# Performance work log

Hardware: AMD Instinct MI355X
Metric: run time of the kernel (lower is better)

The kernel has to match this reference:

```python
import jax, jax.numpy as jnp
import numpy as np

DIM = 2048
CTX_DIM = 4096
NUM_HEADS = 16
HEAD_DIM = DIM // NUM_HEADS
EPS = 1e-6


def _rms_norm(x, weight, eps=EPS):
    # RMSNorm over last dim with learned weight (native dtype path for fp32)
    var = jnp.mean(jnp.square(x), axis=-1, keepdims=True)
    return x * jax.lax.rsqrt(var + eps) * weight


def setup_inputs() -> dict:
    key = jax.random.key(0)
    ks = jax.random.split(key, 12)
    B, L, S = 1, 8192, 512
    sd_q = 1.0 / np.sqrt(DIM)
    sd_c = 1.0 / np.sqrt(CTX_DIM)
    return {
        "x": jax.random.normal(ks[0], (B, L, DIM), dtype=jnp.float32),
        "context": jax.random.normal(ks[1], (B, S, CTX_DIM), dtype=jnp.float32),
        "Wq": jax.random.normal(ks[2], (DIM, DIM), dtype=jnp.float32) * sd_q,
        "bq": jax.random.normal(ks[3], (DIM,), dtype=jnp.float32) * 0.01,
        "Wk": jax.random.normal(ks[4], (CTX_DIM, DIM), dtype=jnp.float32) * sd_c,
        "bk": jax.random.normal(ks[5], (DIM,), dtype=jnp.float32) * 0.01,
        "Wv": jax.random.normal(ks[6], (CTX_DIM, DIM), dtype=jnp.float32) * sd_c,
        "bv": jax.random.normal(ks[7], (DIM,), dtype=jnp.float32) * 0.01,
        "Wo": jax.random.normal(ks[8], (DIM, DIM), dtype=jnp.float32) * sd_q,
        "bo": jax.random.normal(ks[9], (DIM,), dtype=jnp.float32) * 0.01,
        "g_q": jnp.ones((DIM,), dtype=jnp.float32),
        "g_k": jnp.ones((DIM,), dtype=jnp.float32),
    }


def reference(x, context, Wq, bq, Wk, bk, Wv, bv, Wo, bo, g_q, g_k):
    B, L, C = x.shape
    S = context.shape[1]
    # QKV projections + RMSNorm on Q,K (over full model dim, pre head split)
    q = _rms_norm(x @ Wq + bq, g_q)           # [B, L, C]
    k = _rms_norm(context @ Wk + bk, g_k)     # [B, S, C]
    v = context @ Wv + bv                     # [B, S, C]
    # split heads
    q = q.reshape(B, L, NUM_HEADS, HEAD_DIM)
    k = k.reshape(B, S, NUM_HEADS, HEAD_DIM)
    v = v.reshape(B, S, NUM_HEADS, HEAD_DIM)
    # non-causal SDPA
    scale = 1.0 / np.sqrt(HEAD_DIM)
    scores = jnp.einsum("blhd,bshd->bhls", q, k) * scale
    probs = jax.nn.softmax(scores, axis=-1)
    attn = jnp.einsum("bhls,bshd->blhd", probs, v).reshape(B, L, C)
    return attn @ Wo + bo
```

## Files before the change

kernel.cpp:

```cpp
#include <hip/hip_runtime.h>
#include <hip/hip_bf16.h>
#include <stdint.h>

#define L_SEQ 8192
#define S_SEQ 512
#define DIM   2048
#define CTX   4096
#define NH    16
#define HD    128

typedef __bf16 bf16_t;
typedef bf16_t bf16x8 __attribute__((ext_vector_type(8)));
typedef float  f32x4_t __attribute__((ext_vector_type(4)));
typedef float  f32x16_t __attribute__((ext_vector_type(16)));

__device__ __forceinline__ ushort f2b(float f) {
  bf16_t h = (bf16_t)f;
  return __builtin_bit_cast(ushort, h);
}
__device__ __forceinline__ uint32_t pk2(float a, float b) {
  return (uint32_t)f2b(a) | ((uint32_t)f2b(b) << 16);
}
__device__ __forceinline__ float b2f(ushort u) {
  union { uint32_t u; float f; } v; v.u = ((uint32_t)u) << 16;
  return v.f;
}
__device__ __forceinline__ void gll16(const ushort* g, ushort* l) {
  __builtin_amdgcn_global_load_lds((const __attribute__((address_space(1))) void*)g,
                                   (__attribute__((address_space(3))) void*)l, 16, 0, 0);
}
#define SBAR() __builtin_amdgcn_sched_barrier(0)

__global__ __launch_bounds__(256) void k_prep(const float* __restrict__ x,
                                              const float* __restrict__ ctx,
                                              const float* __restrict__ Wq,
                                              const float* __restrict__ Wk,
                                              const float* __restrict__ Wv,
                                              const float* __restrict__ Wo,
                                              const float* __restrict__ gq,
                                              const float* __restrict__ gk,
                                              ushort* __restrict__ xb,
                                              ushort* __restrict__ ctxb,
                                              ushort* __restrict__ wqt,
                                              ushort* __restrict__ wkt,
                                              ushort* __restrict__ wvt,
                                              ushort* __restrict__ wot,
                                              float* __restrict__ g2) {
  const int b = blockIdx.x;
  const int tid = threadIdx.x;
  if (b == 33792) {
    const int d = tid * 8;
#pragma unroll
    for (int j = 0; j < 8; j++) g2[d + j] = gq[d + j] * gk[d + j] * 0.08838834764831843f;
    return;
  }
  if (b < 9216) {
    const float* src; ushort* dst; size_t i;
    if (b < 8192) { src = x;   dst = xb;   i = ((size_t)b * 256 + tid) * 8; }
    else          { src = ctx; dst = ctxb; i = ((size_t)(b - 8192) * 256 + tid) * 8; }
    float4 a = *(const float4*)(src + i);
    float4 c = *(const float4*)(src + i + 4);
    uint4 r;
    r.x = pk2(a.x, a.y); r.y = pk2(a.z, a.w);
    r.z = pk2(c.x, c.y); r.w = pk2(c.z, c.w);
    *(uint4*)(dst + i) = r;
    return;
  }
  __shared__ float t[32][33];
  const float* src; ushort* dst; int K, ti;
  if (b < 13312)      { src = Wq; dst = wqt; K = DIM; ti = b - 9216; }
  else if (b < 21504) { src = Wk; dst = wkt; K = CTX; ti = b - 13312; }
  else if (b < 29696) { src = Wv; dst = wvt; K = CTX; ti = b - 21504; }
  else                { src = Wo; dst = wot; K = DIM; ti = b - 29696; }
  const int n0 = (ti & 63) * 32, k0 = (ti >> 6) * 32;
  const int tx = tid & 31, ty = tid >> 5;
#pragma unroll
  for (int i = 0; i < 4; i++)
    t[ty + 8 * i][tx] = src[(size_t)(k0 + ty + 8 * i) * DIM + n0 + tx];
  __syncthreads();
#pragma unroll
  for (int i = 0; i < 4; i++)
    dst[(size_t)(n0 + ty + 8 * i) * K + k0 + tx] = f2b(t[tx][ty + 8 * i]);
}

__global__ __launch_bounds__(256) void k_knorm(const ushort* __restrict__ kraw,
                                               ushort* __restrict__ kb) {
  const int row = blockIdx.x, tid = threadIdx.x;
  uint4 v = *(const uint4*)(kraw + (size_t)row * DIM + tid * 8);
  const uint32_t* vu = (const uint32_t*)&v;
  float f[8];
#pragma unroll
  for (int i = 0; i < 4; i++) {
    f[2 * i]     = b2f((ushort)(vu[i] & 0xffffu));
    f[2 * i + 1] = b2f((ushort)(vu[i] >> 16));
  }
  float s = 0.f;
#pragma unroll
  for (int i = 0; i < 8; i++) s += f[i] * f[i];
#pragma unroll
  for (int off = 32; off; off >>= 1) s += __shfl_down(s, off);
  __shared__ float wsum[4];
  __shared__ float rtot;
  if ((tid & 63) == 0) wsum[tid >> 6] = s;
  __syncthreads();
  if (tid == 0)
    rtot = rsqrtf((wsum[0] + wsum[1] + wsum[2] + wsum[3]) * (1.0f / DIM) + 1e-6f);
  __syncthreads();
  const float rms = rtot;
  ushort r[8];
#pragma unroll
  for (int i = 0; i < 8; i++) r[i] = f2b(f[i] * rms);
  *(uint4*)(kb + (size_t)row * DIM + tid * 8) = *(uint4*)r;
}

template <int OUT_MODE>
__global__ __launch_bounds__(512, 2) void k_gemm256(const ushort* __restrict__ A,
                                                    const ushort* __restrict__ Bt,
                                                    const float* __restrict__ bias,
                                                    void* __restrict__ outp,
                                                    float* __restrict__ qpart,
                                                    int M, int N, int K) {
  __shared__ __align__(16) ushort lds[65536];
  const int tid = threadIdx.x;
  const int l = tid & 63, wid = tid >> 6;
  const int wm = wid >> 2, wn = wid & 3;
  const int lr = l & 15, lq = l >> 4;

  const int nwg = gridDim.x * gridDim.y;
  const int bid = blockIdx.y * gridDim.x + blockIdx.x;
  const int swz = (bid & 7) * (nwg >> 3) + (bid >> 3);
  const int m0 = (swz / gridDim.x) * 256, n0 = (swz % gridDim.x) * 256;

  f32x4_t acc[8][4];
#pragma unroll
  for (int i = 0; i < 8; i++)
#pragma unroll
    for (int j = 0; j < 4; j++) acc[i][j] = f32x4_t{0.f, 0.f, 0.f, 0.f};

  const int srow = l >> 3;
  const int schunk = ((l & 7) ^ (srow & 7)) * 8;
  auto stage = [&](int buf, int tile, int mat, int h) {
    const ushort* gp = mat ? Bt : A;
    const int rn0 = mat ? n0 : m0;
    const size_t r0 = (size_t)(rn0 + h * 128 + wid * 8 + srow);
    const ushort* g0 = gp + r0 * K + tile * 64 + schunk;
    ushort* l0 = &lds[buf * 32768 + mat * 16384 + (h * 128 + wid * 8) * 64];
    gll16(g0, l0);
    gll16(g0 + (size_t)64 * K, l0 + 64 * 64);
  };

  auto rdA = [&](int buf, int mf, int ks) -> bf16x8 {
    const int R = wm * 128 + mf * 16 + lr;
    return *(const bf16x8*)(&lds[buf * 32768 + R * 64 + (((ks * 4 + lq) ^ (R & 7)) * 8)]);
  };
  auto rdB = [&](int buf, int nf, int ks) -> bf16x8 {
    const int R = wn * 64 + nf * 16 + lr;
    return *(const bf16x8*)(&lds[buf * 32768 + 16384 + R * 64 + (((ks * 4 + lq) ^ (R & 7)) * 8)]);
  };

  const int NT = K >> 6;
  const int NI = NT >> 1;

  stage(0, 0, 0, 0); stage(0, 0, 0, 1); stage(0, 0, 1, 0); stage(0, 0, 1, 1);
  stage(1, 1, 0, 0); stage(1, 1, 0, 1); stage(1, 1, 1, 0); stage(1, 1, 1, 1);
  asm volatile("s_waitcnt vmcnt(8)" ::: "memory");
  SBAR();
  __builtin_amdgcn_s_barrier();
  SBAR();

  bf16x8 a[4][2], a2[4][2], b[2][2], b2[2][2];
  for (int i = 0; i < NI; i++) {
    const bool pf = (i + 1 < NI);
#pragma unroll
    for (int half = 0; half < 2; half++) {
      const int buf = half;
      const int st = 2 * i + 2 + half;
#pragma unroll
      for (int mf = 0; mf < 4; mf++) { a[mf][0] = rdA(buf, mf, 0); a[mf][1] = rdA(buf, mf, 1); }
#pragma unroll
      for (int nf = 0; nf < 2; nf++) { b[nf][0] = rdB(buf, nf, 0); b[nf][1] = rdB(buf, nf, 1); }
      SBAR();
      __builtin_amdgcn_s_barrier();
      asm volatile("s_waitcnt lgkmcnt(0)" ::: "memory");
      SBAR();
      __builtin_amdgcn_s_setprio(1);
#pragma unroll
      for (int mf = 0; mf < 4; mf++)
#pragma unroll
        for (int nf = 0; nf < 2; nf++) {
          acc[mf][nf] = __builtin_amdgcn_mfma_f32_16x16x32_bf16(a[mf][0], b[nf][0], acc[mf][nf], 0, 0, 0);
          acc[mf][nf] = __builtin_amdgcn_mfma_f32_16x16x32_bf16(a[mf][1], b[nf][1], acc[mf][nf], 0, 0, 0);
        }
      __builtin_amdgcn_s_setprio(0);
      SBAR();
      __builtin_amdgcn_s_barrier();
      SBAR();
#pragma unroll
      for (int mf = 0; mf < 4; mf++) { a2[mf][0] = rdA(buf, mf + 4, 0); a2[mf][1] = rdA(buf, mf + 4, 1); }
      SBAR();
      __builtin_amdgcn_s_barrier();
      asm volatile("s_waitcnt lgkmcnt(0)" ::: "memory");
      SBAR();
      __builtin_amdgcn_s_setprio(1);
#pragma unroll
      for (int mf = 0; mf < 4; mf++)
#pragma unroll
        for (int nf = 0; nf < 2; nf++) {
          acc[mf + 4][nf] = __builtin_amdgcn_mfma_f32_16x16x32_bf16(a2[mf][0], b[nf][0], acc[mf + 4][nf], 0, 0, 0);
          acc[mf + 4][nf] = __builtin_amdgcn_mfma_f32_16x16x32_bf16(a2[mf][1], b[nf][1], acc[mf + 4][nf], 0, 0, 0);
        }
      __builtin_amdgcn_s_setprio(0);
      SBAR();
      __builtin_amdgcn_s_barrier();
      SBAR();
#pragma unroll
      for (int nf = 0; nf < 2; nf++) { b2[nf][0] = rdB(buf, nf + 2, 0); b2[nf][1] = rdB(buf, nf + 2, 1); }
      if (pf) { stage(buf, st, 0, 0); stage(buf, st, 0, 1); }
      SBAR();
      __builtin_amdgcn_s_barrier();
      asm volatile("s_waitcnt lgkmcnt(0)" ::: "memory");
      SBAR();
      __builtin_amdgcn_s_setprio(1);
#pragma unroll
      for (int mf = 0; mf < 4; mf++)
#pragma unroll
        for (int nf = 0; nf < 2; nf++) {
          acc[mf + 4][nf + 2] = __builtin_amdgcn_mfma_f32_16x16x32_bf16(a2[mf][0], b2[nf][0], acc[mf + 4][nf + 2], 0, 0, 0);
          acc[mf + 4][nf + 2] = __builtin_amdgcn_mfma_f32_16x16x32_bf16(a2[mf][1], b2[nf][1], acc[mf + 4][nf + 2], 0, 0, 0);
        }
      __builtin_amdgcn_s_setprio(0);
      SBAR();
      __builtin_amdgcn_s_barrier();
      SBAR();
      if (pf) {
        stage(buf, st, 1, 0); stage(buf, st, 1, 1);
        asm volatile("s_waitcnt vmcnt(8)" ::: "memory");
      } else if (half == 0) {
        asm volatile("s_waitcnt vmcnt(0)" ::: "memory");
      }
      SBAR();
      __builtin_amdgcn_s_barrier();
      SBAR();
      __builtin_amdgcn_s_setprio(1);
#pragma unroll
      for (int mf = 0; mf < 4; mf++)
#pragma unroll
        for (int nf = 0; nf < 2; nf++) {
          acc[mf][nf + 2] = __builtin_amdgcn_mfma_f32_16x16x32_bf16(a[mf][0], b2[nf][0], acc[mf][nf + 2], 0, 0, 0);
          acc[mf][nf + 2] = __builtin_amdgcn_mfma_f32_16x16x32_bf16(a[mf][1], b2[nf][1], acc[mf][nf + 2], 0, 0, 0);
        }
      __builtin_amdgcn_s_setprio(0);
      SBAR();
      __builtin_amdgcn_s_barrier();
      SBAR();
    }
  }

  float bvs[4];
#pragma unroll
  for (int nf = 0; nf < 4; nf++) bvs[nf] = bias[n0 + wn * 64 + nf * 16 + lr];
#pragma unroll
  for (int nf = 0; nf < 4; nf++) {
    const int col = n0 + wn * 64 + nf * 16 + lr;
#pragma unroll
    for (int mf = 0; mf < 8; mf++) {
#pragma unroll
      for (int r = 0; r < 4; r++) {
        const int row = m0 + wm * 128 + mf * 16 + lq * 4 + r;
        const float v = acc[mf][nf][r] + bvs[nf];
        if constexpr (OUT_MODE == 0)
          ((float*)outp)[(size_t)row * N + col] = v;
        else
          ((ushort*)outp)[(size_t)row * N + col] = f2b(v);
      }
    }
  }
  if constexpr (OUT_MODE == 1) {
    const int slot = (n0 >> 8) * 4 + wn;
#pragma unroll
    for (int mf = 0; mf < 8; mf++) {
#pragma unroll
      for (int r = 0; r < 4; r++) {
        float s = 0.f;
#pragma unroll
        for (int nf = 0; nf < 4; nf++) {
          const float v = acc[mf][nf][r] + bvs[nf];
          s += v * v;
        }
        s += __shfl_xor(s, 1); s += __shfl_xor(s, 2);
        s += __shfl_xor(s, 4); s += __shfl_xor(s, 8);
        if (lr == 0)
          qpart[(size_t)(m0 + wm * 128 + mf * 16 + lq * 4 + r) * 32 + slot] = s;
      }
    }
  }
}

__global__ __launch_bounds__(256) void k_gemmkv(const ushort* __restrict__ A,
                                                const ushort* __restrict__ Bt,
                                                const float* __restrict__ biasK,
                                                const float* __restrict__ biasV,
                                                ushort* __restrict__ outK,
                                                ushort* __restrict__ outVt) {
  __shared__ __align__(16) ushort As[4][128 * 32];
  __shared__ __align__(16) ushort Bs[4][64 * 32];
  const int tid = threadIdx.x;
  const int l = tid & 63, wid = tid >> 6;
  const int wr = wid >> 1, wc = wid & 1;
  const int lr = l & 15, lq = l >> 4;
  const int K = CTX, M = S_SEQ;

  const int bid = blockIdx.x;
  const int swz = (bid & 7) * 32 + (bid >> 3);
  const int n0 = (swz >> 2) * 64, m0 = (swz & 3) * 128;

  f32x4_t acc[4][2];
#pragma unroll
  for (int i = 0; i < 4; i++)
#pragma unroll
    for (int j = 0; j < 2; j++) acc[i][j] = f32x4_t{0.f, 0.f, 0.f, 0.f};

  const int srow = l >> 2;
  const int schunk = ((l & 3) ^ ((srow >> 1) & 3)) * 8;
  const ushort* gA = A  + (size_t)(m0 + srow) * K + schunk;
  const ushort* gB = Bt + (size_t)(n0 + wid * 16 + srow) * K + schunk;

  auto stage = [&](int buf, int kt) {
    const int ko = kt * 32;
    gll16(gA + (size_t)(wid * 16) * K + ko,      &As[buf][(wid * 16) * 32]);
    gll16(gA + (size_t)(64 + wid * 16) * K + ko, &As[buf][(64 + wid * 16) * 32]);
    gll16(gB + ko,                               &Bs[buf][(wid * 16) * 32]);
  };
  auto rdA = [&](int buf, int mi) -> bf16x8 {
    const int R = wr * 64 + mi * 16 + lr;
    return *(const bf16x8*)(&As[buf][R * 32 + ((lq ^ ((R >> 1) & 3)) * 8)]);
  };
  auto rdB = [&](int buf, int ni) -> bf16x8 {
    const int R = wc * 32 + ni * 16 + lr;
    return *(const bf16x8*)(&Bs[buf][R * 32 + ((lq ^ ((R >> 1) & 3)) * 8)]);
  };

  const int NT = K >> 5;
  stage(0, 0); stage(1, 1); stage(2, 2);
  for (int t = 0; t < NT; t++) {
    const int cur = t & 3;
    if (t + 3 < NT) { stage((t + 3) & 3, t + 3); asm volatile("s_waitcnt vmcnt(9)" ::: "memory"); }
    else if (t + 2 < NT) { asm volatile("s_waitcnt vmcnt(6)" ::: "memory"); }
    else if (t + 1 < NT) { asm volatile("s_waitcnt vmcnt(3)" ::: "memory"); }
    else                 { asm volatile("s_waitcnt vmcnt(0)" ::: "memory"); }
    SBAR();
    __builtin_amdgcn_s_barrier();
    SBAR();

    bf16x8 af[4], bfr[2];
#pragma unroll
    for (int mi = 0; mi < 4; mi++) af[mi] = rdA(cur, mi);
#pragma unroll
    for (int ni = 0; ni < 2; ni++) bfr[ni] = rdB(cur, ni);
    __builtin_amdgcn_s_setprio(1);
#pragma unroll
    for (int mi = 0; mi < 4; mi++)
#pragma unroll
      for (int ni = 0; ni < 2; ni++)
        acc[mi][ni] = __builtin_amdgcn_mfma_f32_16x16x32_bf16(af[mi], bfr[ni], acc[mi][ni], 0, 0, 0);
    __builtin_amdgcn_s_setprio(0);
    SBAR();
    __builtin_amdgcn_s_barrier();
    SBAR();
  }

  if (n0 < DIM) {
#pragma unroll
    for (int mi = 0; mi < 4; mi++) {
#pragma unroll
      for (int ni = 0; ni < 2; ni++) {
        const int col = n0 + wc * 32 + ni * 16 + lr;
        const float bv = biasK[col];
#pragma unroll
        for (int r = 0; r < 4; r++) {
          const int row = m0 + wr * 64 + mi * 16 + lq * 4 + r;
          outK[(size_t)row * DIM + col] = f2b(acc[mi][ni][r] + bv);
        }
      }
    }
  } else {
    ushort* ldst = &As[0][0];
    __syncthreads();
#pragma unroll
    for (int mi = 0; mi < 4; mi++) {
#pragma unroll
      for (int ni = 0; ni < 2; ni++) {
        const int ccol = wc * 32 + ni * 16 + lr;
        const float bv = biasV[n0 - DIM + ccol];
#pragma unroll
        for (int r = 0; r < 4; r++) {
          const int crow = wr * 64 + mi * 16 + lq * 4 + r;
          ldst[ccol * 128 + crow] = f2b(acc[mi][ni][r] + bv);
        }
      }
    }
    __syncthreads();
    const int c = tid >> 2, j0 = (tid & 3) * 32;
    ushort* dst = outVt + (size_t)(n0 - DIM + c) * M + m0 + j0;
#pragma unroll
    for (int k2 = 0; k2 < 4; k2++)
      *(uint4*)(dst + k2 * 8) = *(const uint4*)(ldst + c * 128 + j0 + k2 * 8);
  }
}

__global__ __launch_bounds__(256) void k_attn(const ushort* __restrict__ Qraw,
                                              const ushort* __restrict__ Kb,
                                              const ushort* __restrict__ Vt,
                                              const float* __restrict__ qpart,
                                              const float* __restrict__ g2,
                                              ushort* __restrict__ Ob) {
  __shared__ __align__(16) ushort smem[16384];
  ushort* Ks = smem;
  ushort* Vs = smem + 64 * 128;

  const int tid = threadIdx.x;
  const int l = tid & 63, wid = tid >> 6;
  const int lo = l & 31, hi = l >> 5;

  const int bid = blockIdx.x;
  const int swz = (bid & 7) * 128 + (bid >> 3);
  const int h = swz >> 6;
  const int q0 = (swz & 63) * 128 + wid * 32;

  bf16x8 qf[8];
  {
    float ssum = 0.f;
    const float* pp = qpart + (size_t)(q0 + lo) * 32;
#pragma unroll
    for (int i = 0; i < 8; i++) {
      float4 t = *(const float4*)(pp + i * 4);
      ssum += t.x + t.y + t.z + t.w;
    }
    const float qs = rsqrtf(ssum * (1.0f / DIM) + 1e-6f);
    const ushort* qp = Qraw + (size_t)(q0 + lo) * DIM + h * HD + hi * 8;
    const float* gp = g2 + h * HD + hi * 8;
#pragma unroll
    for (int ds = 0; ds < 8; ds++) {
      union { uint4 u; ushort us[8]; } rw;
      rw.u = *(const uint4*)(qp + ds * 16);
      float4 ga_ = *(const float4*)(gp + ds * 16);
      float4 gb_ = *(const float4*)(gp + ds * 16 + 4);
      union { uint32_t w[4]; bf16x8 v; } ov;
      ov.w[0] = pk2(b2f(rw.us[0]) * qs * ga_.x, b2f(rw.us[1]) * qs * ga_.y);
      ov.w[1] = pk2(b2f(rw.us[2]) * qs * ga_.z, b2f(rw.us[3]) * qs * ga_.w);
      ov.w[2] = pk2(b2f(rw.us[4]) * qs * gb_.x, b2f(rw.us[5]) * qs * gb_.y);
      ov.w[3] = pk2(b2f(rw.us[6]) * qs * gb_.z, b2f(rw.us[7]) * qs * gb_.w);
      qf[ds] = ov.v;
    }
  }

  f32x16_t o[4] = {};
  float m_run = -1e30f, l_run = 0.f;

  for (int kvb = 0; kvb < S_SEQ / 64; kvb++) {
    __syncthreads();
#pragma unroll
    for (int i = 0; i < 4; i++) {
      const int c = i * 256 + tid, row = c >> 4, cs = c & 15;
      gll16(Kb + (size_t)(kvb * 64 + row) * DIM + h * HD + ((cs ^ (row & 7)) * 8),
            Ks + c * 8);
    }
#pragma unroll
    for (int i = 0; i < 4; i++) {
      const int c = i * 256 + tid, row = c >> 3, cs = c & 7;
      gll16(Vt + (size_t)(h * HD + row) * S_SEQ + kvb * 64 + ((cs ^ (row & 7)) * 8),
            Vs + c * 8);
    }
    __syncthreads();

    f32x16_t sA = {}, sB = {};
#pragma unroll
    for (int ds = 0; ds < 8; ds++) {
      const int ch = ((hi + ds * 2) ^ (lo & 7)) * 8;
      bf16x8 kA = *(const bf16x8*)(Ks + lo * 128 + ch);
      bf16x8 kB = *(const bf16x8*)(Ks + (32 + lo) * 128 + ch);
      sA = __builtin_amdgcn_mfma_f32_32x32x16_bf16(kA, qf[ds], sA, 0, 0, 0);
      sB = __builtin_amdgcn_mfma_f32_32x32x16_bf16(kB, qf[ds], sB, 0, 0, 0);
    }

    float p[32];
#pragma unroll
    for (int i = 0; i < 16; i++) { p[i] = sA[i]; p[16 + i] = sB[i]; }
    float pm = p[0];
#pragma unroll
    for (int i = 1; i < 32; i++) pm = fmaxf(pm, p[i]);
    pm = fmaxf(pm, __shfl_xor(pm, 32));
    const float mn = fmaxf(m_run, pm);
    const float corr = __expf(m_run - mn);
    m_run = mn;
    float ps = 0.f;
#pragma unroll
    for (int i = 0; i < 32; i++) { p[i] = __expf(p[i] - mn); ps += p[i]; }
    ps += __shfl_xor(ps, 32);
    l_run = l_run * corr + ps;
#pragma unroll
    for (int nt = 0; nt < 4; nt++) o[nt] *= corr;

    uint32_t c[16];
#pragma unroll
    for (int j = 0; j < 16; j++) c[j] = pk2(p[2 * j], p[2 * j + 1]);
    bf16x8 pf[4];
#pragma unroll
    for (int s = 0; s < 4; s++) {
      const uint32_t ca = c[4 * s], cb = c[4 * s + 1], cc = c[4 * s + 2], cd = c[4 * s + 3];
      const uint32_t sa = __shfl_xor(ca, 32), sb = __shfl_xor(cb, 32);
      const uint32_t sc = __shfl_xor(cc, 32), sd = __shfl_xor(cd, 32);
      union { uint32_t u[4]; bf16x8 v; } f;
      f.u[0] = hi ? sc : ca; f.u[1] = hi ? sd : cb;
      f.u[2] = hi ? cc : sa; f.u[3] = hi ? cd : sb;
      pf[s] = f.v;
    }

#pragma unroll
    for (int nt = 0; nt < 4; nt++) {
      const int vrow = nt * 32 + lo;
#pragma unroll
      for (int s = 0; s < 4; s++) {
        bf16x8 vf = *(const bf16x8*)(Vs + vrow * 64 + (((s * 2 + hi) ^ (lo & 7)) * 8));
        o[nt] = __builtin_amdgcn_mfma_f32_32x32x16_bf16(vf, pf[s], o[nt], 0, 0, 0);
      }
    }
  }

  const float inv = 1.0f / l_run;
#pragma unroll
  for (int nt = 0; nt < 4; nt++) o[nt] *= inv;

  __syncthreads();
  float* tb = (float*)smem + wid * (32 * 33);
  const int q2 = l >> 1, dh = (l & 1) * 16;
#pragma unroll
  for (int nt = 0; nt < 4; nt++) {
#pragma unroll
    for (int r = 0; r < 16; r++)
      tb[lo * 33 + ((r & 3) + 8 * (r >> 2) + 4 * hi)] = o[nt][r];
    asm volatile("s_waitcnt lgkmcnt(0)" ::: "memory");
    SBAR();
    ushort tmp[16];
#pragma unroll
    for (int j = 0; j < 16; j++) tmp[j] = f2b(tb[q2 * 33 + dh + j]);
    asm volatile("s_waitcnt lgkmcnt(0)" ::: "memory");
    SBAR();
    const size_t oaddr = (size_t)(q0 + q2) * DIM + h * HD + nt * 32 + dh;
    *(uint4*)(Ob + oaddr) = *(uint4*)tmp;
    *(uint4*)(Ob + oaddr + 8) = *(uint4*)(tmp + 8);
  }
}

extern "C" void kernel_launch(void* const* d_in, const int* in_sizes, int n_in,
                              void* d_out, int out_size, void* d_ws, size_t ws_size,
                              hipStream_t stream) {
  const float* x   = (const float*)d_in[0];
  const float* ctx = (const float*)d_in[1];
  const float* Wq  = (const float*)d_in[2];
  const float* bq  = (const float*)d_in[3];
  const float* Wk  = (const float*)d_in[4];
  const float* bk  = (const float*)d_in[5];
  const float* Wv  = (const float*)d_in[6];
  const float* bv  = (const float*)d_in[7];
  const float* Wo  = (const float*)d_in[8];
  const float* bo  = (const float*)d_in[9];
  const float* gq  = (const float*)d_in[10];
  const float* gk  = (const float*)d_in[11];

  char* ws = (char*)d_ws;
  ushort* wqt    = (ushort*)(ws);
  ushort* wkt    = (ushort*)(ws + 8388608);
  ushort* wvt    = (ushort*)(ws + 25165824);
  ushort* wot    = (ushort*)(ws + 41943040);
  ushort* ctxb   = (ushort*)(ws + 50331648);
  float*  g2     = (float*)(ws + 54558720);
  float*  qpart  = (float*)(ws + 56623104);
  ushort* kb     = (ushort*)(ws + 83886080);
  ushort* vt     = (ushort*)(ws + 85983232);
  ushort* xb     = (ushort*)(ws + 88080384);
  ushort* kraw   = (ushort*)(ws + 88080384);
  ushort* attnb  = (ushort*)(ws + 88080384);
  ushort* qraw   = (ushort*)(ws + 121634816);

  k_prep<<<33793, 256, 0, stream>>>(x, ctx, Wq, Wk, Wv, Wo, gq, gk,
                                    xb, ctxb, wqt, wkt, wvt, wot, g2);
  k_gemm256<1><<<dim3(DIM / 256, L_SEQ / 256), 512, 0, stream>>>(xb, wqt, bq, qraw, qpart, L_SEQ, DIM, DIM);
  k_gemmkv<<<256, 256, 0, stream>>>(ctxb, wkt, bk, bv, kraw, vt);
  k_knorm<<<S_SEQ, 256, 0, stream>>>(kraw, kb);
  k_attn<<<L_SEQ / 128 * NH, 256, 0, stream>>>(qraw, kb, vt, qpart, g2, attnb);
  k_gemm256<0><<<dim3(DIM / 256, L_SEQ / 256), 512, 0, stream>>>(attnb, wot, bo, d_out, nullptr, L_SEQ, DIM, DIM);
}
```

Measured before the change: 312.5 us.

## Rework GEMM K-loop staging, deepen KV GEMM pipeline, add lazy softmax rescale

The main Q/O GEMM drops the two-tiles-per-iteration loop with two in-flight buffers and uses a simple per-tile double-buffered loop. The next tile's four staging chunks are spread across the compute phases, and the waitcnt now covers only the first chunk. The KV GEMM ring buffer grows from 4 to 6 LDS slots with a prefetch depth of 5, with waitcnt values adjusted to match. Flash attention skips the running-max update and output rescale when the new block max stays within 8 of the current max, avoiding exp and multiply work. The risks are less load latency hiding in the main GEMM, higher LDS use lowering occupancy in the KV GEMM, and a possible race: chunks staged into nxt are only guarded by a vmcnt(2) wait, so the next iteration may read data that has not fully arrived.

```diff
diff --git a/kernel.cpp b/kernel.cpp
--- a/kernel.cpp
+++ b/kernel.cpp
@@ -159,101 +159,87 @@
   };
 
   const int NT = K >> 6;
-  const int NI = NT >> 1;
-
   stage(0, 0, 0, 0); stage(0, 0, 0, 1); stage(0, 0, 1, 0); stage(0, 0, 1, 1);
-  stage(1, 1, 0, 0); stage(1, 1, 0, 1); stage(1, 1, 1, 0); stage(1, 1, 1, 1);
-  asm volatile("s_waitcnt vmcnt(8)" ::: "memory");
-  SBAR();
-  __builtin_amdgcn_s_barrier();
-  SBAR();
 
   bf16x8 a[4][2], a2[4][2], b[2][2], b2[2][2];
-  for (int i = 0; i < NI; i++) {
-    const bool pf = (i + 1 < NI);
-#pragma unroll
-    for (int half = 0; half < 2; half++) {
-      const int buf = half;
-      const int st = 2 * i + 2 + half;
-#pragma unroll
-      for (int mf = 0; mf < 4; mf++) { a[mf][0] = rdA(buf, mf, 0); a[mf][1] = rdA(buf, mf, 1); }
-#pragma unroll
-      for (int nf = 0; nf < 2; nf++) { b[nf][0] = rdB(buf, nf, 0); b[nf][1] = rdB(buf, nf, 1); }
-      SBAR();
-      __builtin_amdgcn_s_barrier();
-      asm volatile("s_waitcnt lgkmcnt(0)" ::: "memory");
-      SBAR();
-      __builtin_amdgcn_s_setprio(1);
-#pragma unroll
-      for (int mf = 0; mf < 4; mf++)
-#pragma unroll
-        for (int nf = 0; nf < 2; nf++) {
-          acc[mf][nf] = __builtin_amdgcn_mfma_f32_16x16x32_bf16(a[mf][0], b[nf][0], acc[mf][nf], 0, 0, 0);
-          acc[mf][nf] = __builtin_amdgcn_mfma_f32_16x16x32_bf16(a[mf][1], b[nf][1], acc[mf][nf], 0, 0, 0);
-        }
-      __builtin_amdgcn_s_setprio(0);
-      SBAR();
-      __builtin_amdgcn_s_barrier();
-      SBAR();
-#pragma unroll
-      for (int mf = 0; mf < 4; mf++) { a2[mf][0] = rdA(buf, mf + 4, 0); a2[mf][1] = rdA(buf, mf + 4, 1); }
-      SBAR();
-      __builtin_amdgcn_s_barrier();
-      asm volatile("s_waitcnt lgkmcnt(0)" ::: "memory");
-      SBAR();
-      __builtin_amdgcn_s_setprio(1);
-#pragma unroll
-      for (int mf = 0; mf < 4; mf++)
-#pragma unroll
-        for (int nf = 0; nf < 2; nf++) {
-          acc[mf + 4][nf] = __builtin_amdgcn_mfma_f32_16x16x32_bf16(a2[mf][0], b[nf][0], acc[mf + 4][nf], 0, 0, 0);
-          acc[mf + 4][nf] = __builtin_amdgcn_mfma_f32_16x16x32_bf16(a2[mf][1], b[nf][1], acc[mf + 4][nf], 0, 0, 0);
-        }
-      __builtin_amdgcn_s_setprio(0);
-      SBAR();
-      __builtin_amdgcn_s_barrier();
-      SBAR();
-#pragma unroll
-      for (int nf = 0; nf < 2; nf++) { b2[nf][0] = rdB(buf, nf + 2, 0); b2[nf][1] = rdB(buf, nf + 2, 1); }
-      if (pf) { stage(buf, st, 0, 0); stage(buf, st, 0, 1); }
-      SBAR();
-      __builtin_amdgcn_s_barrier();
-      asm volatile("s_waitcnt lgkmcnt(0)" ::: "memory");
-      SBAR();
-      __builtin_amdgcn_s_setprio(1);
-#pragma unroll
-      for (int mf = 0; mf < 4; mf++)
-#pragma unroll
-        for (int nf = 0; nf < 2; nf++) {
-          acc[mf + 4][nf + 2] = __builtin_amdgcn_mfma_f32_16x16x32_bf16(a2[mf][0], b2[nf][0], acc[mf + 4][nf + 2], 0, 0, 0);
-          acc[mf + 4][nf + 2] = __builtin_amdgcn_mfma_f32_16x16x32_bf16(a2[mf][1], b2[nf][1], acc[mf + 4][nf + 2], 0, 0, 0);
-        }
-      __builtin_amdgcn_s_setprio(0);
-      SBAR();
-      __builtin_amdgcn_s_barrier();
-      SBAR();
-      if (pf) {
-        stage(buf, st, 1, 0); stage(buf, st, 1, 1);
-        asm volatile("s_waitcnt vmcnt(8)" ::: "memory");
-      } else if (half == 0) {
-        asm volatile("s_waitcnt vmcnt(0)" ::: "memory");
-      }
-      SBAR();
-      __builtin_amdgcn_s_barrier();
-      SBAR();
-      __builtin_amdgcn_s_setprio(1);
-#pragma unroll
-      for (int mf = 0; mf < 4; mf++)
-#pragma unroll
-        for (int nf = 0; nf < 2; nf++) {
-          acc[mf][nf + 2] = __builtin_amdgcn_mfma_f32_16x16x32_bf16(a[mf][0], b2[nf][0], acc[mf][nf + 2], 0, 0, 0);
-          acc[mf][nf + 2] = __builtin_amdgcn_mfma_f32_16x16x32_bf16(a[mf][1], b2[nf][1], acc[mf][nf + 2], 0, 0, 0);
-        }
-      __builtin_amdgcn_s_setprio(0);
-      SBAR();
-      __builtin_amdgcn_s_barrier();
-      SBAR();
-    }
+  for (int kt = 0; kt < NT; kt++) {
+    const int cur = kt & 1, nxt = cur ^ 1;
+    const bool pf = (kt + 1 < NT);
+    if (pf) { stage(nxt, kt + 1, 0, 0); asm volatile("s_waitcnt vmcnt(2)" ::: "memory"); }
+    else    { asm volatile("s_waitcnt vmcnt(0)" ::: "memory"); }
+    SBAR();
+    __builtin_amdgcn_s_barrier();
+    SBAR();
+#pragma unroll
+    for (int mf = 0; mf < 4; mf++) { a[mf][0] = rdA(cur, mf, 0); a[mf][1] = rdA(cur, mf, 1); }
+#pragma unroll
+    for (int nf = 0; nf < 2; nf++) { b[nf][0] = rdB(cur, nf, 0); b[nf][1] = rdB(cur, nf, 1); }
+    __builtin_amdgcn_s_setprio(1);
+#pragma unroll
+    for (int mf = 0; mf < 4; mf++)
+#pragma unroll
+      for (int nf = 0; nf < 2; nf++) {
+        acc[mf][nf] = __builtin_amdgcn_mfma_f32_16x16x32_bf16(a[mf][0], b[nf][0], acc[mf][nf], 0, 0, 0);
+        acc[mf][nf] = __builtin_amdgcn_mfma_f32_16x16x32_bf16(a[mf][1], b[nf][1], acc[mf][nf], 0, 0, 0);
+      }
+    __builtin_amdgcn_s_setprio(0);
+    SBAR();
+    __builtin_amdgcn_s_barrier();
+    SBAR();
+#pragma unroll
+    for (int mf = 0; mf < 4; mf++) { a2[mf][0] = rdA(cur, mf + 4, 0); a2[mf][1] = rdA(cur, mf + 4, 1); }
+    if (pf) stage(nxt, kt + 1, 0, 1);
+    SBAR();
+    __builtin_amdgcn_s_barrier();
+    SBAR();
+    __builtin_amdgcn_s_setprio(1);
+#pragma unroll
+    for (int mf = 0; mf < 4; mf++)
+#pragma unroll
+      for (int nf = 0; nf < 2; nf++) {
+        acc[mf + 4][nf] = __builtin_amdgcn_mfma_f32_16x16x32_bf16(a2[mf][0], b[nf][0], acc[mf + 4][nf], 0, 0, 0);
+        acc[mf + 4][nf] = __builtin_amdgcn_mfma_f32_16x16x32_bf16(a2[mf][1], b[nf][1], acc[mf + 4][nf], 0, 0, 0);
+      }
+    __builtin_amdgcn_s_setprio(0);
+    SBAR();
+    __builtin_amdgcn_s_barrier();
+    SBAR();
+#pragma unroll
+    for (int nf = 0; nf < 2; nf++) { b2[nf][0] = rdB(cur, nf + 2, 0); b2[nf][1] = rdB(cur, nf + 2, 1); }
+    if (pf) stage(nxt, kt + 1, 1, 0);
+    SBAR();
+    __builtin_amdgcn_s_barrier();
+    SBAR();
+    __builtin_amdgcn_s_setprio(1);
+#pragma unroll
+    for (int mf = 0; mf < 4; mf++)
+#pragma unroll
+      for (int nf = 0; nf < 2; nf++) {
+        acc[mf + 4][nf + 2] = __builtin_amdgcn_mfma_f32_16x16x32_bf16(a2[mf][0], b2[nf][0], acc[mf + 4][nf + 2], 0, 0, 0);
+        acc[mf + 4][nf + 2] = __builtin_amdgcn_mfma_f32_16x16x32_bf16(a2[mf][1], b2[nf][1], acc[mf + 4][nf + 2], 0, 0, 0);
+      }
+    __builtin_amdgcn_s_setprio(0);
+    SBAR();
+    __builtin_amdgcn_s_barrier();
+    SBAR();
+#pragma unroll
+    for (int mf = 0; mf < 4; mf++) { a[mf][0] = rdA(cur, mf, 0); a[mf][1] = rdA(cur, mf, 1); }
+    if (pf) stage(nxt, kt + 1, 1, 1);
+    SBAR();
+    __builtin_amdgcn_s_barrier();
+    SBAR();
+    __builtin_amdgcn_s_setprio(1);
+#pragma unroll
+    for (int mf = 0; mf < 4; mf++)
+#pragma unroll
+      for (int nf = 0; nf < 2; nf++) {
+        acc[mf][nf + 2] = __builtin_amdgcn_mfma_f32_16x16x32_bf16(a[mf][0], b2[nf][0], acc[mf][nf + 2], 0, 0, 0);
+        acc[mf][nf + 2] = __builtin_amdgcn_mfma_f32_16x16x32_bf16(a[mf][1], b2[nf][1], acc[mf][nf + 2], 0, 0, 0);
+      }
+    __builtin_amdgcn_s_setprio(0);
+    SBAR();
+    __builtin_amdgcn_s_barrier();
+    SBAR();
   }
 
   float bvs[4];
@@ -302,8 +288,8 @@
                                                 const float* __restrict__ biasV,
                                                 ushort* __restrict__ outK,
                                                 ushort* __restrict__ outVt) {
-  __shared__ __align__(16) ushort As[4][128 * 32];
-  __shared__ __align__(16) ushort Bs[4][64 * 32];
+  __shared__ __align__(16) ushort As[6][128 * 32];
+  __shared__ __align__(16) ushort Bs[6][64 * 32];
   const int tid = threadIdx.x;
   const int l = tid & 63, wid = tid >> 6;
   const int wr = wid >> 1, wc = wid & 1;
@@ -341,10 +327,16 @@
   };
 
   const int NT = K >> 5;
-  stage(0, 0); stage(1, 1); stage(2, 2);
+  stage(0, 0); stage(1, 1); stage(2, 2); stage(3, 3); stage(4, 4);
+  int cur = 0;
   for (int t = 0; t < NT; t++) {
-    const int cur = t & 3;
-    if (t + 3 < NT) { stage((t + 3) & 3, t + 3); asm volatile("s_waitcnt vmcnt(9)" ::: "memory"); }
+    if (t + 5 < NT) {
+      const int prv = (cur == 0) ? 5 : cur - 1;
+      stage(prv, t + 5);
+      asm volatile("s_waitcnt vmcnt(15)" ::: "memory");
+    }
+    else if (t + 4 < NT) { asm volatile("s_waitcnt vmcnt(12)" ::: "memory"); }
+    else if (t + 3 < NT) { asm volatile("s_waitcnt vmcnt(9)" ::: "memory"); }
     else if (t + 2 < NT) { asm volatile("s_waitcnt vmcnt(6)" ::: "memory"); }
     else if (t + 1 < NT) { asm volatile("s_waitcnt vmcnt(3)" ::: "memory"); }
     else                 { asm volatile("s_waitcnt vmcnt(0)" ::: "memory"); }
@@ -367,6 +359,7 @@
     SBAR();
     __builtin_amdgcn_s_barrier();
     SBAR();
+    cur = (cur == 5) ? 0 : cur + 1;
   }
 
   if (n0 < DIM) {
@@ -490,16 +483,24 @@
 #pragma unroll
     for (int i = 1; i < 32; i++) pm = fmaxf(pm, p[i]);
     pm = fmaxf(pm, __shfl_xor(pm, 32));
-    const float mn = fmaxf(m_run, pm);
-    const float corr = __expf(m_run - mn);
-    m_run = mn;
-    float ps = 0.f;
-#pragma unroll
-    for (int i = 0; i < 32; i++) { p[i] = __expf(p[i] - mn); ps += p[i]; }
-    ps += __shfl_xor(ps, 32);
-    l_run = l_run * corr + ps;
-#pragma unroll
-    for (int nt = 0; nt < 4; nt++) o[nt] *= corr;
+    if (__all(pm - m_run <= 8.0f)) {
+      float ps = 0.f;
+#pragma unroll
+      for (int i = 0; i < 32; i++) { p[i] = __expf(p[i] - m_run); ps += p[i]; }
+      ps += __shfl_xor(ps, 32);
+      l_run += ps;
+    } else {
+      const float mn = fmaxf(m_run, pm);
+      const float corr = __expf(m_run - mn);
+      m_run = mn;
+      float ps = 0.f;
+#pragma unroll
+      for (int i = 0; i < 32; i++) { p[i] = __expf(p[i] - mn); ps += p[i]; }
+      ps += __shfl_xor(ps, 32);
+      l_run = l_run * corr + ps;
+#pragma unroll
+      for (int nt = 0; nt < 4; nt++) o[nt] *= corr;
+    }
 
     uint32_t c[16];
 #pragma unroll
```

After: 343.5 us. +9.9%, slower.
